# Optimization experiments

Measured on AMD Instinct MI355X. Metric: run time of the kernel, lower is better.

Reference implementation:

```python
import jax, jax.numpy as jnp
import numpy as np

N = 100000
E = 600000
DIM = 128
EDGE_DIM = 32

def setup_inputs() -> dict:
    key = jax.random.key(0)
    ks = jax.random.split(key, 10)
    s = 1.0 / np.sqrt(DIM)
    se = 1.0 / np.sqrt(EDGE_DIM)
    return {
        "x": jax.random.normal(ks[0], (N, DIM), dtype=jnp.float32),
        "edge_index": jax.random.randint(ks[1], (2, E), 0, N, dtype=jnp.int64),
        "edge_attr": jax.random.normal(ks[2], (E, EDGE_DIM), dtype=jnp.float32),
        "We": jax.random.uniform(ks[3], (EDGE_DIM, DIM), minval=-se, maxval=se, dtype=jnp.float32),
        "be": jnp.zeros((DIM,), dtype=jnp.float32),
        "W1": jax.random.uniform(ks[4], (DIM, DIM), minval=-s, maxval=s, dtype=jnp.float32),
        "b1": jnp.zeros((DIM,), dtype=jnp.float32),
        "W2": jax.random.uniform(ks[5], (DIM, DIM), minval=-s, maxval=s, dtype=jnp.float32),
        "b2": jnp.zeros((DIM,), dtype=jnp.float32),
        "eps": jnp.float32(0.0),
        "gamma": jnp.ones((DIM,), dtype=jnp.float32),
        "beta": jnp.zeros((DIM,), dtype=jnp.float32),
    }

def reference(x, edge_index, edge_attr, We, be, W1, b1, W2, b2, eps, gamma, beta):
    i, j = edge_index[0], edge_index[1]
    # gather source node features and add transformed edge features -> [E, dim]
    msg = x[j] + (edge_attr @ We + be)
    # scatter-sum aggregate to destination nodes -> [N, dim]
    agg = jax.ops.segment_sum(msg, i, num_segments=x.shape[0])
    h = (1.0 + eps) * x + agg
    # 2-layer MLP
    out = jax.nn.relu(h @ W1 + b1) @ W2 + b2
    # LayerNorm over last dim (dropout is identity in eval)
    mu = jnp.mean(out, axis=-1, keepdims=True)
    var = jnp.var(out, axis=-1, keepdims=True)
    out = (out - mu) * jax.lax.rsqrt(var + 1e-5) * gamma + beta
    return out
```

## Files before the change

### kernel.cpp

```cpp
#include <hip/hip_runtime.h>
#include <hip/hip_bf16.h>

#define N_NODES 100000
#define N_EDGES 600000
#define DIM 128
#define EDIM 32

typedef __attribute__((ext_vector_type(8))) short bf16x8;
typedef __attribute__((ext_vector_type(4))) float f32x4;

static __device__ __forceinline__ short f2bf(float v) {
    __hip_bfloat16 h = __float2bfloat16(v);
    return *(short*)&h;
}
static __device__ __forceinline__ float bfu2f(unsigned short u) {
    return __uint_as_float(((unsigned int)u) << 16);
}

#define AGGX_OFF  0ULL
#define AGGE_OFF  25600000ULL
#define CSR_OFF   32000000ULL
#define OFF_OFF   36800000ULL
#define DEG_OFF   37200008ULL
#define BSUM_OFF  37600016ULL
#define WEW1_OFF  37600528ULL
#define SCAN_NBLK 98

__global__ __launch_bounds__(1024) void compute_wew1(
    const float* __restrict__ We, const float* __restrict__ W1,
    float* __restrict__ wew1) {
    const int idx = blockIdx.x * 1024 + threadIdx.x;
    const int k = idx >> 7, d2 = idx & 127;
    float a = 0.f;
    #pragma unroll 8
    for (int d = 0; d < DIM; ++d)
        a += We[k * DIM + d] * W1[d * DIM + d2];
    wew1[k * DIM + d2] = a;
}

__global__ void count_deg(const int* __restrict__ eidx, int* __restrict__ deg) {
    int e = blockIdx.x * 256 + threadIdx.x;
    if (e < N_EDGES) atomicAdd(&deg[eidx[e]], 1);
}

__global__ __launch_bounds__(1024) void scan_blocks(
    const int* __restrict__ deg, int* __restrict__ off, int* __restrict__ bsum) {
    const int t = blockIdx.x * 1024 + threadIdx.x;
    const int lane = threadIdx.x & 63, wv = threadIdx.x >> 6;
    int v = (t < N_NODES) ? deg[t] : 0;
    int s = v;
    #pragma unroll
    for (int o = 1; o < 64; o <<= 1) {
        int u = __shfl_up(s, o, 64);
        if (lane >= o) s += u;
    }
    __shared__ int wsum[16];
    if (lane == 63) wsum[wv] = s;
    __syncthreads();
    if (threadIdx.x == 0) {
        int a = 0;
        #pragma unroll
        for (int w = 0; w < 16; ++w) { int tmp = wsum[w]; wsum[w] = a; a += tmp; }
        bsum[blockIdx.x] = a;
    }
    __syncthreads();
    if (t < N_NODES) off[t] = s - v + wsum[wv];
}

__global__ void scan_totals(int* __restrict__ bsum) {
    if (threadIdx.x == 0) {
        int a = 0;
        for (int i = 0; i < SCAN_NBLK; ++i) { int t = bsum[i]; bsum[i] = a; a += t; }
    }
}

__global__ __launch_bounds__(1024) void scan_add(int* __restrict__ off, const int* __restrict__ bsum) {
    const int t = blockIdx.x * 1024 + threadIdx.x;
    if (t < N_NODES) off[t] += bsum[blockIdx.x];
}

__global__ void csr_fill(const int* __restrict__ eidx, int* __restrict__ off,
                         int2* __restrict__ csr) {
    int e = blockIdx.x * 256 + threadIdx.x;
    if (e < N_EDGES) {
        int i = eidx[e];
        int p = atomicAdd(&off[i], 1);
        csr[p] = make_int2(e, eidx[N_EDGES + e]);
    }
}

__global__ __launch_bounds__(256) void gine_aggregate(
    const float* __restrict__ x,
    const float* __restrict__ eattr,
    const int* __restrict__ off_end,
    const int* __restrict__ deg,
    const int2* __restrict__ csr,
    unsigned short* __restrict__ aggX,
    unsigned short* __restrict__ aggE)
{
    const int lane = threadIdx.x & 63;
    const int gw = (blockIdx.x * 256 + threadIdx.x) >> 6;
    const int nw = (gridDim.x * 256) >> 6;

    for (int n = gw; n < N_NODES; n += nw) {
        const int dg = deg[n];
        const int s = off_end[n] - dg;
        float a0 = 0.f, a1 = 0.f, ae = 0.f;

        for (int t0 = 0; t0 < dg; t0 += 8) {
            const int c = min(8, dg - t0);
            int ei[8], ji[8];
            #pragma unroll
            for (int k = 0; k < 8; ++k)
                if (k < c) { int2 cc = csr[s + t0 + k]; ei[k] = cc.x; ji[k] = cc.y; }
            float xv0[8], xv1[8], ev[8];
            #pragma unroll
            for (int k = 0; k < 8; ++k)
                if (k < c) {
                    xv0[k] = x[(size_t)ji[k] * DIM + lane];
                    xv1[k] = x[(size_t)ji[k] * DIM + 64 + lane];
                    ev[k]  = (lane < 32) ? eattr[(size_t)ei[k] * EDIM + lane] : 0.f;
                }
            #pragma unroll
            for (int k = 0; k < 8; ++k)
                if (k < c) { a0 += xv0[k]; a1 += xv1[k]; ae += ev[k]; }
        }
        aggX[(size_t)n * DIM + lane]      = (unsigned short)f2bf(a0);
        aggX[(size_t)n * DIM + 64 + lane] = (unsigned short)f2bf(a1);
        if (lane < 32) aggE[(size_t)n * EDIM + lane] = (unsigned short)f2bf(ae);
    }
}

#define HROW_STRIDE 136

__global__ __launch_bounds__(1024) void gine_mlp_fused(
    const float* __restrict__ x,
    const unsigned short* __restrict__ aggX,
    const unsigned short* __restrict__ aggE,
    const int* __restrict__ deg,
    const float* __restrict__ wew1,
    const float* __restrict__ be,
    const float* __restrict__ W1,
    const float* __restrict__ b1,
    const float* __restrict__ W2,
    const float* __restrict__ b2,
    const float* __restrict__ epsp,
    const float* __restrict__ gamma,
    const float* __restrict__ beta,
    float* __restrict__ out)
{
    __shared__ short Wp[2][16384];
    __shared__ short Wep[4096];
    __shared__ short hrow[16][16 * HROW_STRIDE];

    const int tid  = threadIdx.x;
    const int wave = tid >> 6;
    const int lane = tid & 63;
    const int m    = lane & 15;
    const int g    = lane >> 4;

    for (int s = wave * 2; s < wave * 2 + 2; ++s) {
        const int dt = s >> 2, kc = s & 3;
        const int krow = kc * 32 + g * 8;
        const int col  = dt * 16 + m;
        short p1[8], p2[8];
        #pragma unroll
        for (int j = 0; j < 8; ++j) {
            p1[j] = f2bf(W1[(size_t)(krow + j) * DIM + col]);
            p2[j] = f2bf(W2[(size_t)(krow + j) * DIM + col]);
        }
        #pragma unroll
        for (int j = 0; j < 8; ++j) {
            Wp[0][(s * 64 + lane) * 8 + j] = p1[j];
            Wp[1][(s * 64 + lane) * 8 + j] = p2[j];
        }
    }
    if (wave < 8) {
        const int dt = wave;
        const int col = dt * 16 + m;
        short pw[8];
        #pragma unroll
        for (int j = 0; j < 8; ++j) pw[j] = f2bf(wew1[(size_t)(g * 8 + j) * DIM + col]);
        #pragma unroll
        for (int j = 0; j < 8; ++j) Wep[(dt * 64 + lane) * 8 + j] = pw[j];
    }

    float b1v[8], b2v[8], gv[8], btv[8];
    #pragma unroll
    for (int dt = 0; dt < 8; ++dt) {
        const int d = dt * 16 + m;
        b1v[dt] = b1[d]; b2v[dt] = b2[d]; gv[dt] = gamma[d]; btv[dt] = beta[d];
    }
    const float epv = 1.0f + epsp[0];
    __syncthreads();

    short* myrow = &hrow[wave][0];
    const int ntiles = N_NODES / 16;

    for (int tile = blockIdx.x * 16 + wave; tile < ntiles; tile += gridDim.x * 16) {
        const int nbase = tile * 16;

        bf16x8 afragE = *(const bf16x8*)&aggE[(size_t)(nbase + m) * EDIM + g * 8];

        #pragma unroll
        for (int r = 0; r < 8; ++r) {
            const int idx4 = r * 64 + lane;
            const int node = idx4 >> 5, dq = idx4 & 31;
            const size_t goff = (size_t)(nbase + node) * DIM + dq * 4;
            float4 xv = *(const float4*)&x[goff];
            ushort4 au = *(const ushort4*)&aggX[goff];
            float4 bev = ((const float4*)be)[dq];
            float dgf = (float)deg[nbase + node];
            short4 hv;
            hv.x = f2bf(epv * xv.x + bfu2f(au.x) + dgf * bev.x);
            hv.y = f2bf(epv * xv.y + bfu2f(au.y) + dgf * bev.y);
            hv.z = f2bf(epv * xv.z + bfu2f(au.z) + dgf * bev.z);
            hv.w = f2bf(epv * xv.w + bfu2f(au.w) + dgf * bev.w);
            *(short4*)&myrow[node * HROW_STRIDE + dq * 4] = hv;
        }
        __asm__ volatile("s_waitcnt lgkmcnt(0)" ::: "memory");

        f32x4 acc[8];
        #pragma unroll
        for (int dt = 0; dt < 8; ++dt) {
            bf16x8 bfrag = *(bf16x8*)&Wep[(dt * 64 + lane) * 8];
            acc[dt] = __builtin_amdgcn_mfma_f32_16x16x32_bf16(
                afragE, bfrag, (f32x4){0.f, 0.f, 0.f, 0.f}, 0, 0, 0);
        }
        #pragma unroll
        for (int kc = 0; kc < 4; ++kc) {
            bf16x8 afrag = *(bf16x8*)&myrow[m * HROW_STRIDE + kc * 32 + g * 8];
            #pragma unroll
            for (int dt = 0; dt < 8; ++dt) {
                bf16x8 bfrag = *(bf16x8*)&Wp[0][((dt * 4 + kc) * 64 + lane) * 8];
                acc[dt] = __builtin_amdgcn_mfma_f32_16x16x32_bf16(afrag, bfrag, acc[dt], 0, 0, 0);
            }
        }
        __asm__ volatile("s_waitcnt lgkmcnt(0)" ::: "memory");

        #pragma unroll
        for (int dt = 0; dt < 8; ++dt)
            #pragma unroll
            for (int q = 0; q < 4; ++q) {
                float v = fmaxf(acc[dt][q] + b1v[dt], 0.f);
                myrow[(g * 4 + q) * HROW_STRIDE + dt * 16 + m] = f2bf(v);
            }
        __asm__ volatile("s_waitcnt lgkmcnt(0)" ::: "memory");

        #pragma unroll
        for (int dt = 0; dt < 8; ++dt) acc[dt] = (f32x4){0.f, 0.f, 0.f, 0.f};
        #pragma unroll
        for (int kc = 0; kc < 4; ++kc) {
            bf16x8 afrag = *(bf16x8*)&myrow[m * HROW_STRIDE + kc * 32 + g * 8];
            #pragma unroll
            for (int dt = 0; dt < 8; ++dt) {
                bf16x8 bfrag = *(bf16x8*)&Wp[1][((dt * 4 + kc) * 64 + lane) * 8];
                acc[dt] = __builtin_amdgcn_mfma_f32_16x16x32_bf16(afrag, bfrag, acc[dt], 0, 0, 0);
            }
        }

        float s[4] = {0, 0, 0, 0}, ss[4] = {0, 0, 0, 0};
        #pragma unroll
        for (int dt = 0; dt < 8; ++dt)
            #pragma unroll
            for (int q = 0; q < 4; ++q) {
                float o = acc[dt][q] + b2v[dt];
                acc[dt][q] = o;
                s[q] += o; ss[q] += o * o;
            }
        #pragma unroll
        for (int mask = 1; mask < 16; mask <<= 1)
            #pragma unroll
            for (int q = 0; q < 4; ++q) {
                s[q]  += __shfl_xor(s[q], mask, 64);
                ss[q] += __shfl_xor(ss[q], mask, 64);
            }
        float mu[4], inv[4];
        #pragma unroll
        for (int q = 0; q < 4; ++q) {
            mu[q] = s[q] * (1.0f / DIM);
            float var = ss[q] * (1.0f / DIM) - mu[q] * mu[q];
            inv[q] = rsqrtf(var + 1e-5f);
        }
        #pragma unroll
        for (int dt = 0; dt < 8; ++dt)
            #pragma unroll
            for (int q = 0; q < 4; ++q) {
                const int node = nbase + g * 4 + q;
                out[(size_t)node * DIM + dt * 16 + m] =
                    (acc[dt][q] - mu[q]) * inv[q] * gv[dt] + btv[dt];
            }
    }
}

extern "C" void kernel_launch(void* const* d_in, const int* in_sizes, int n_in,
                              void* d_out, int out_size, void* d_ws, size_t ws_size,
                              hipStream_t stream) {
    const float* x     = (const float*)d_in[0];
    const int*   eidx  = (const int*)d_in[1];
    const float* eattr = (const float*)d_in[2];
    const float* We    = (const float*)d_in[3];
    const float* be    = (const float*)d_in[4];
    const float* W1    = (const float*)d_in[5];
    const float* b1    = (const float*)d_in[6];
    const float* W2    = (const float*)d_in[7];
    const float* b2v   = (const float*)d_in[8];
    const float* eps   = (const float*)d_in[9];
    const float* gamma = (const float*)d_in[10];
    const float* beta  = (const float*)d_in[11];
    float* out = (float*)d_out;

    char* ws = (char*)d_ws;
    unsigned short* aggX = (unsigned short*)(ws + AGGX_OFF);
    unsigned short* aggE = (unsigned short*)(ws + AGGE_OFF);
    int2*  csr  = (int2*)(ws + CSR_OFF);
    int*   off  = (int*)(ws + OFF_OFF);
    int*   deg  = (int*)(ws + DEG_OFF);
    int*   bsum = (int*)(ws + BSUM_OFF);
    float* wew1 = (float*)(ws + WEW1_OFF);

    hipMemsetAsync(deg, 0, 400000, stream);
    compute_wew1<<<4, 1024, 0, stream>>>(We, W1, wew1);
    count_deg<<<(N_EDGES + 255) / 256, 256, 0, stream>>>(eidx, deg);
    scan_blocks<<<SCAN_NBLK, 1024, 0, stream>>>(deg, off, bsum);
    scan_totals<<<1, 64, 0, stream>>>(bsum);
    scan_add<<<SCAN_NBLK, 1024, 0, stream>>>(off, bsum);
    csr_fill<<<(N_EDGES + 255) / 256, 256, 0, stream>>>(eidx, off, csr);
    gine_aggregate<<<2048, 256, 0, stream>>>(x, eattr, off, deg, csr, aggX, aggE);
    gine_mlp_fused<<<256, 1024, 0, stream>>>(x, aggX, aggE, deg, wew1, be,
                                             W1, b1, W2, b2v, eps, gamma, beta, out);
}
```

Measured before the change: 359.4 us.

## Use half-wave per node with float4 gathers and merge scan kernels

Aggregation now assigns 32 lanes per node with float4 loads of x, so each wave handles two nodes and has more independent gathers in flight. The next node's CSR bounds are prefetched. The scan totals and add kernels are merged into one that reduces block sums in parallel and writes a separate cursor, so the offsets array keeps start positions and degree comes from adjacent offsets. This removes one launch and the deg reads, in exchange for a larger per-lane register footprint.

New measurement: 351.4 us. 2.2% less time.

```diff
diff --git a/kernel.cpp b/kernel.cpp
--- a/kernel.cpp
+++ b/kernel.cpp
@@ -38,16 +38,16 @@
     wew1[k * DIM + d2] = a;
 }
 
-__global__ void count_deg(const int* __restrict__ eidx, int* __restrict__ deg) {
+__global__ void count_deg(const int* __restrict__ eidx, int* __restrict__ cnt) {
     int e = blockIdx.x * 256 + threadIdx.x;
-    if (e < N_EDGES) atomicAdd(&deg[eidx[e]], 1);
+    if (e < N_EDGES) atomicAdd(&cnt[eidx[e]], 1);
 }
 
 __global__ __launch_bounds__(1024) void scan_blocks(
-    const int* __restrict__ deg, int* __restrict__ off, int* __restrict__ bsum) {
+    const int* __restrict__ cnt, int* __restrict__ off, int* __restrict__ bsum) {
     const int t = blockIdx.x * 1024 + threadIdx.x;
     const int lane = threadIdx.x & 63, wv = threadIdx.x >> 6;
-    int v = (t < N_NODES) ? deg[t] : 0;
+    int v = (t < N_NODES) ? cnt[t] : 0;
     int s = v;
     #pragma unroll
     for (int o = 1; o < 64; o <<= 1) {
@@ -67,67 +67,86 @@
     if (t < N_NODES) off[t] = s - v + wsum[wv];
 }
 
-__global__ void scan_totals(int* __restrict__ bsum) {
-    if (threadIdx.x == 0) {
-        int a = 0;
-        for (int i = 0; i < SCAN_NBLK; ++i) { int t = bsum[i]; bsum[i] = a; a += t; }
-    }
-}
-
-__global__ __launch_bounds__(1024) void scan_add(int* __restrict__ off, const int* __restrict__ bsum) {
-    const int t = blockIdx.x * 1024 + threadIdx.x;
-    if (t < N_NODES) off[t] += bsum[blockIdx.x];
-}
-
-__global__ void csr_fill(const int* __restrict__ eidx, int* __restrict__ off,
+__global__ __launch_bounds__(1024) void scan_add2(
+    int* __restrict__ off, int* __restrict__ cursor, const int* __restrict__ bsum) {
+    __shared__ int pref;
+    const int b = blockIdx.x;
+    if (threadIdx.x < 64) {
+        int v = 0;
+        if ((int)threadIdx.x < b) v = bsum[threadIdx.x];
+        const int i2 = threadIdx.x + 64;
+        if (i2 < b) v += bsum[i2];
+        #pragma unroll
+        for (int o = 32; o >= 1; o >>= 1) v += __shfl_down(v, o, 64);
+        if (threadIdx.x == 0) pref = v;
+    }
+    __syncthreads();
+    const int t = b * 1024 + threadIdx.x;
+    if (t < N_NODES) {
+        const int val = off[t] + pref;
+        off[t] = val;
+        cursor[t] = val;
+    } else if (t == N_NODES) {
+        off[t] = N_EDGES;
+    }
+}
+
+__global__ void csr_fill(const int* __restrict__ eidx, int* __restrict__ cursor,
                          int2* __restrict__ csr) {
     int e = blockIdx.x * 256 + threadIdx.x;
     if (e < N_EDGES) {
         int i = eidx[e];
-        int p = atomicAdd(&off[i], 1);
+        int p = atomicAdd(&cursor[i], 1);
         csr[p] = make_int2(e, eidx[N_EDGES + e]);
     }
 }
 
-__global__ __launch_bounds__(256) void gine_aggregate(
+__global__ __launch_bounds__(256, 4) void gine_aggregate(
     const float* __restrict__ x,
     const float* __restrict__ eattr,
-    const int* __restrict__ off_end,
-    const int* __restrict__ deg,
+    const int* __restrict__ off,
     const int2* __restrict__ csr,
     unsigned short* __restrict__ aggX,
     unsigned short* __restrict__ aggE)
 {
-    const int lane = threadIdx.x & 63;
-    const int gw = (blockIdx.x * 256 + threadIdx.x) >> 6;
-    const int nw = (gridDim.x * 256) >> 6;
-
-    for (int n = gw; n < N_NODES; n += nw) {
-        const int dg = deg[n];
-        const int s = off_end[n] - dg;
-        float a0 = 0.f, a1 = 0.f, ae = 0.f;
-
-        for (int t0 = 0; t0 < dg; t0 += 8) {
-            const int c = min(8, dg - t0);
-            int ei[8], ji[8];
+    const int l5 = threadIdx.x & 31;
+    const int nhw = (gridDim.x * 256) >> 5;
+    int n = (blockIdx.x * 256 + threadIdx.x) >> 5;
+
+    int s = off[n], e = off[n + 1];
+    while (true) {
+        const int n2 = n + nhw;
+        int s2 = 0, e2 = 0;
+        if (n2 < N_NODES) { s2 = off[n2]; e2 = off[n2 + 1]; }
+
+        float a0 = 0.f, a1 = 0.f, a2 = 0.f, a3 = 0.f, ae = 0.f;
+        for (int t0 = s; t0 < e; t0 += 8) {
+            const int c = e - t0;
+            int ji[8], ei[8];
             #pragma unroll
             for (int k = 0; k < 8; ++k)
-                if (k < c) { int2 cc = csr[s + t0 + k]; ei[k] = cc.x; ji[k] = cc.y; }
-            float xv0[8], xv1[8], ev[8];
+                if (k < c) { int2 cc = csr[t0 + k]; ei[k] = cc.x; ji[k] = cc.y; }
+            float4 xv[8]; float ev[8];
             #pragma unroll
             for (int k = 0; k < 8; ++k)
                 if (k < c) {
-                    xv0[k] = x[(size_t)ji[k] * DIM + lane];
-                    xv1[k] = x[(size_t)ji[k] * DIM + 64 + lane];
-                    ev[k]  = (lane < 32) ? eattr[(size_t)ei[k] * EDIM + lane] : 0.f;
+                    xv[k] = *(const float4*)&x[(size_t)ji[k] * DIM + l5 * 4];
+                    ev[k] = eattr[(size_t)ei[k] * EDIM + l5];
                 }
             #pragma unroll
             for (int k = 0; k < 8; ++k)
-                if (k < c) { a0 += xv0[k]; a1 += xv1[k]; ae += ev[k]; }
-        }
-        aggX[(size_t)n * DIM + lane]      = (unsigned short)f2bf(a0);
-        aggX[(size_t)n * DIM + 64 + lane] = (unsigned short)f2bf(a1);
-        if (lane < 32) aggE[(size_t)n * EDIM + lane] = (unsigned short)f2bf(ae);
+                if (k < c) {
+                    a0 += xv[k].x; a1 += xv[k].y; a2 += xv[k].z; a3 += xv[k].w;
+                    ae += ev[k];
+                }
+        }
+        short4 hv;
+        hv.x = f2bf(a0); hv.y = f2bf(a1); hv.z = f2bf(a2); hv.w = f2bf(a3);
+        *(short4*)&aggX[(size_t)n * DIM + l5 * 4] = hv;
+        aggE[(size_t)n * EDIM + l5] = (unsigned short)f2bf(ae);
+
+        if (n2 >= N_NODES) break;
+        n = n2; s = s2; e = e2;
     }
 }
 
@@ -137,7 +156,7 @@
     const float* __restrict__ x,
     const unsigned short* __restrict__ aggX,
     const unsigned short* __restrict__ aggE,
-    const int* __restrict__ deg,
+    const int* __restrict__ off,
     const float* __restrict__ wew1,
     const float* __restrict__ be,
     const float* __restrict__ W1,
@@ -210,7 +229,7 @@
             float4 xv = *(const float4*)&x[goff];
             ushort4 au = *(const ushort4*)&aggX[goff];
             float4 bev = ((const float4*)be)[dq];
-            float dgf = (float)deg[nbase + node];
+            float dgf = (float)(off[nbase + node + 1] - off[nbase + node]);
             short4 hv;
             hv.x = f2bf(epv * xv.x + bfu2f(au.x) + dgf * bev.x);
             hv.y = f2bf(epv * xv.y + bfu2f(au.y) + dgf * bev.y);
@@ -315,18 +334,17 @@
     unsigned short* aggE = (unsigned short*)(ws + AGGE_OFF);
     int2*  csr  = (int2*)(ws + CSR_OFF);
     int*   off  = (int*)(ws + OFF_OFF);
-    int*   deg  = (int*)(ws + DEG_OFF);
+    int*   cnt  = (int*)(ws + DEG_OFF);
     int*   bsum = (int*)(ws + BSUM_OFF);
     float* wew1 = (float*)(ws + WEW1_OFF);
 
-    hipMemsetAsync(deg, 0, 400000, stream);
+    hipMemsetAsync(cnt, 0, 400000, stream);
     compute_wew1<<<4, 1024, 0, stream>>>(We, W1, wew1);
-    count_deg<<<(N_EDGES + 255) / 256, 256, 0, stream>>>(eidx, deg);
-    scan_blocks<<<SCAN_NBLK, 1024, 0, stream>>>(deg, off, bsum);
-    scan_totals<<<1, 64, 0, stream>>>(bsum);
-    scan_add<<<SCAN_NBLK, 1024, 0, stream>>>(off, bsum);
-    csr_fill<<<(N_EDGES + 255) / 256, 256, 0, stream>>>(eidx, off, csr);
-    gine_aggregate<<<2048, 256, 0, stream>>>(x, eattr, off, deg, csr, aggX, aggE);
-    gine_mlp_fused<<<256, 1024, 0, stream>>>(x, aggX, aggE, deg, wew1, be,
+    count_deg<<<(N_EDGES + 255) / 256, 256, 0, stream>>>(eidx, cnt);
+    scan_blocks<<<SCAN_NBLK, 1024, 0, stream>>>(cnt, off, bsum);
+    scan_add2<<<SCAN_NBLK, 1024, 0, stream>>>(off, cnt, bsum);
+    csr_fill<<<(N_EDGES + 255) / 256, 256, 0, stream>>>(eidx, cnt, csr);
+    gine_aggregate<<<2048, 256, 0, stream>>>(x, eattr, off, csr, aggX, aggE);
+    gine_mlp_fused<<<256, 1024, 0, stream>>>(x, aggX, aggE, off, wew1, be,
                                              W1, b1, W2, b2v, eps, gamma, beta, out);
 }
```
